# Kernel tuning notes

Hardware: AMD Instinct MI355X
Metric: run time of the kernel (lower is better)

## Reference

```python
import jax, jax.numpy as jnp
import numpy as np

N_NODES = 100000
N_EDGES = 1600000
D_IN = 128
UNITS = 128


def setup_inputs() -> dict:
    key = jax.random.key(0)
    k1, k2, k3, k4, k5 = jax.random.split(key, 5)
    x = jax.random.normal(k1, (N_NODES, D_IN), dtype=jnp.float32)
    # glorot-uniform-like dense weight
    limit = float(np.sqrt(6.0 / (D_IN + UNITS)))
    w = jax.random.uniform(k2, (D_IN, UNITS), minval=-limit, maxval=limit, dtype=jnp.float32)
    # COO sparse adjacency: A[row, col] = val
    edge_row = jax.random.randint(k3, (N_EDGES,), 0, N_NODES, dtype=jnp.int32)
    edge_col = jax.random.randint(k4, (N_EDGES,), 0, N_NODES, dtype=jnp.int32)
    edge_val = jax.random.uniform(k5, (N_EDGES,), dtype=jnp.float32)
    return {"x": x, "w": w, "edge_row": edge_row, "edge_col": edge_col, "edge_val": edge_val}


def reference(x, w, edge_row, edge_col, edge_val):
    # dropout rate = 0.0 -> identity (module default)
    xw = x @ w                                   # [N, units] dense projection
    # sparse adjacency propagation: out[i] = sum_e val[e] * xw[col[e]] for row[e]==i
    msgs = xw[edge_col] * edge_val[:, None]      # [E, units] irregular gather
    out = jax.ops.segment_sum(msgs, edge_row, num_segments=x.shape[0])
    return jax.nn.relu(out)                      # activation
```

## Files before the change

### kernel.cpp

```cpp
#include <hip/hip_runtime.h>

#define N_NODES 100000
#define N_EDGES 1600000
#define D 128
#define NB 512
#define BCAP 3584
#define BSTRIDE 16
#define CHUNK 4000
#define NSCAT 400
#define NGEMMB 521
#define NTILES 1563
#define HCAPQ 1024
#define CTS 132

typedef __attribute__((ext_vector_type(8))) short  short8;
typedef __attribute__((ext_vector_type(4))) float  floatx4;

__device__ __forceinline__ ushort f2bf(float f) {
    unsigned u = __float_as_uint(f);
    u += 0x7FFF + ((u >> 16) & 1);
    return (ushort)(u >> 16);
}
__device__ __forceinline__ float bf2f(ushort s) {
    return __uint_as_float((unsigned)s << 16);
}
__device__ __forceinline__ int bucket_of(int r)  { return (int)(((unsigned)r << 9) / 100000u); }
__device__ __forceinline__ int row_start(int b)  { return (b * 100000 + 511) >> 9; }

union SMem {
    struct {
        int2  stage[CHUNK];
        int   sA[NB];
        int   sB[NB];
        int   lcur[NB];
        int   gbase[NB];
        short sbuck[CHUNK];
    } sc;
    struct {
        ushort wt[128 * 128];
        ushort ct[4][16 * CTS];
    } ge;
};

__global__ __launch_bounds__(256) void gemm_and_scatter(const float* __restrict__ x,
                                                        const float* __restrict__ w,
                                                        ushort* __restrict__ xwb,
                                                        const int* __restrict__ erow,
                                                        const int* __restrict__ ecol,
                                                        const float* __restrict__ eval,
                                                        int* __restrict__ bcnt,
                                                        int2* __restrict__ bkt) {
    __shared__ SMem sm;
    const int t = threadIdx.x;

    if (blockIdx.x < NGEMMB) {
        ushort* wt = sm.ge.wt;
        const int wv   = t >> 6;
        const int lane = t & 63;
        const int m    = lane & 15;
        const int q    = lane >> 4;

        {
            const float4* w4 = (const float4*)w;
            for (int i = t; i < 4096; i += 256) {
                const float4 v = w4[i];
                const int k = i >> 5;
                const int n = (i & 31) << 2;
                const int c = k >> 3, kc = k & 7;
#pragma unroll
                for (int d = 0; d < 4; ++d) {
                    const float val = (d == 0) ? v.x : (d == 1) ? v.y : (d == 2) ? v.z : v.w;
                    const int nn = n + d;
                    wt[(nn << 7) | (((c ^ (nn & 15)) & 15) << 3) | kc] = f2bf(val);
                }
            }
        }
        __syncthreads();

        float4 xa[8];
        {
            const int rb0 = blockIdx.x * 64 + wv * 16;
            const float* xr = x + (size_t)min(rb0 + m, N_NODES - 1) * D + q * 8;
#pragma unroll
            for (int k2 = 0; k2 < 4; ++k2) {
                xa[k2 * 2 + 0] = *(const float4*)(xr + k2 * 32);
                xa[k2 * 2 + 1] = *(const float4*)(xr + k2 * 32 + 4);
            }
        }

        for (int tb = blockIdx.x; tb < NTILES; tb += NGEMMB) {
            const int rbase = tb * 64 + wv * 16;

            short8 afr[4];
#pragma unroll
            for (int k2 = 0; k2 < 4; ++k2) {
                const float4 a0 = xa[k2 * 2 + 0];
                const float4 a1 = xa[k2 * 2 + 1];
                short8 a;
                a[0] = (short)f2bf(a0.x); a[1] = (short)f2bf(a0.y);
                a[2] = (short)f2bf(a0.z); a[3] = (short)f2bf(a0.w);
                a[4] = (short)f2bf(a1.x); a[5] = (short)f2bf(a1.y);
                a[6] = (short)f2bf(a1.z); a[7] = (short)f2bf(a1.w);
                afr[k2] = a;
            }

            const int tnext = tb + NGEMMB;
            if (tnext < NTILES) {
                const int rbn = tnext * 64 + wv * 16;
                const float* xr = x + (size_t)min(rbn + m, N_NODES - 1) * D + q * 8;
#pragma unroll
                for (int k2 = 0; k2 < 4; ++k2) {
                    xa[k2 * 2 + 0] = *(const float4*)(xr + k2 * 32);
                    xa[k2 * 2 + 1] = *(const float4*)(xr + k2 * 32 + 4);
                }
            }

            floatx4 acc[8];
#pragma unroll
            for (int tt = 0; tt < 8; ++tt) acc[tt] = (floatx4){0.f, 0.f, 0.f, 0.f};

#pragma unroll
            for (int k2 = 0; k2 < 4; ++k2) {
#pragma unroll
                for (int tt = 0; tt < 8; ++tt) {
                    const int n  = tt * 16 + m;
                    const int cc = (((k2 << 2) + q) ^ m) & 15;
                    const short8 b = *(const short8*)&wt[(n << 7) | (cc << 3)];
                    acc[tt] = __builtin_amdgcn_mfma_f32_16x16x32_bf16(afr[k2], b, acc[tt], 0, 0, 0);
                }
            }

#pragma unroll
            for (int tt = 0; tt < 8; ++tt) {
#pragma unroll
                for (int r = 0; r < 4; ++r) {
                    sm.ge.ct[wv][((q << 2) | r) * CTS + tt * 16 + m] = f2bf(acc[tt][r]);
                }
            }
            const int rl  = lane >> 2;
            const int ch  = lane & 3;
            const int row = rbase + rl;
            if (row < N_NODES) {
                const ushort* srcp = &sm.ge.ct[wv][rl * CTS + ch * 32];
                ushort*       dstp = &xwb[(size_t)row * D + ch * 32];
#pragma unroll
                for (int u = 0; u < 4; ++u) {
                    ((int4*)dstp)[u] = ((const int4*)srcp)[u];
                }
            }
        }
    } else {
        const int e0 = (blockIdx.x - NGEMMB) * CHUNK;
        int*   sA    = sm.sc.sA;
        int*   sB    = sm.sc.sB;
        int*   lcur  = sm.sc.lcur;
        int*   gbase = sm.sc.gbase;
        short* sbuck = sm.sc.sbuck;
        int2*  stage = sm.sc.stage;

        sA[t] = 0; sA[t + 256] = 0;
        __syncthreads();

        for (int i = t; i < CHUNK; i += 256) {
            atomicAdd(&sA[bucket_of(erow[e0 + i])], 1);
        }
        __syncthreads();

        int cur = 0;
        int* bufs[2] = {sA, sB};
#pragma unroll
        for (int o = 1; o < 512; o <<= 1) {
            const int* src = bufs[cur];
            int*       dst = bufs[cur ^ 1];
            const int i0 = t, i1 = t + 256;
            dst[i0] = src[i0] + ((i0 >= o) ? src[i0 - o] : 0);
            dst[i1] = src[i1] + ((i1 >= o) ? src[i1 - o] : 0);
            cur ^= 1;
            __syncthreads();
        }
        {
            const int* incl = bufs[cur];
            int*       excl = bufs[cur ^ 1];
            excl[t]       = (t == 0) ? 0 : incl[t - 1];
            excl[t + 256] = incl[t + 255];
        }
        __syncthreads();
        int* L = bufs[cur ^ 1];

        for (int b = t; b < NB; b += 256) {
            lcur[b] = L[b];
            const int cnt = ((b == NB - 1) ? CHUNK : L[b + 1]) - L[b];
            gbase[b] = (cnt > 0) ? atomicAdd(&bcnt[b * BSTRIDE], cnt) : 0;
        }
        __syncthreads();

        for (int i = t; i < CHUNK; i += 256) {
            const int   r = erow[e0 + i];
            const int   c = ecol[e0 + i];
            const float v = eval[e0 + i];
            const int   b = bucket_of(r);
            const int  rl = r - row_start(b);
            const int pos = atomicAdd(&lcur[b], 1);
            stage[pos] = make_int2((rl << 17) | c, __float_as_int(v));
            sbuck[pos] = (short)b;
        }
        __syncthreads();

        for (int i = t; i < CHUNK; i += 256) {
            const int b   = sbuck[i];
            const int dst = gbase[b] + (i - L[b]);
            if (dst < BCAP) bkt[(size_t)b * BCAP + dst] = stage[i];
        }
    }
}

__global__ __launch_bounds__(256, 4) void csr_gather(const int* __restrict__ bcnt,
                                                     const int2* __restrict__ bkt,
                                                     const ushort* __restrict__ xwb,
                                                     float* __restrict__ out,
                                                     int b0) {
    __shared__ int2 lcsr[HCAPQ];
    __shared__ int  sA[256], sB[256], lcur[256];
    const int b  = b0 + (blockIdx.x >> 2);
    const int qh = blockIdx.x & 3;
    const int t  = threadIdx.x;
    const int n  = min(bcnt[b * BSTRIDE], BCAP);
    const int r0    = row_start(b);
    const int nrows = row_start(b + 1) - r0;
    const int lo    = (nrows * qh) >> 2;
    const int hi    = (nrows * (qh + 1)) >> 2;
    const int nloc  = hi - lo;

    const int2* src = bkt + (size_t)b * BCAP;
    sA[t] = 0;
    __syncthreads();

    for (int i = t; i < n; i += 256) {
        const int rl = (int)(((unsigned)src[i].x) >> 17);
        if (rl >= lo && rl < hi) atomicAdd(&sA[rl - lo], 1);
    }
    __syncthreads();

    int cur = 0;
    int* bufs[2] = {sA, sB};
#pragma unroll
    for (int o = 1; o < 256; o <<= 1) {
        const int* s = bufs[cur];
        int*       d = bufs[cur ^ 1];
        d[t] = s[t] + ((t >= o) ? s[t - o] : 0);
        cur ^= 1;
        __syncthreads();
    }
    lcur[t] = (t == 0) ? 0 : bufs[cur][t - 1];
    __syncthreads();

    for (int i = t; i < n; i += 256) {
        const int2 e = src[i];
        const int rl = (int)(((unsigned)e.x) >> 17);
        if (rl >= lo && rl < hi) {
            const int pos = atomicAdd(&lcur[rl - lo], 1);
            if (pos < HCAPQ) lcsr[pos] = make_int2(e.x & 0x1FFFF, e.y);
        }
    }
    __syncthreads();

    const int qid = t >> 4;
    const int lc  = (t & 15) << 3;

    for (int ln = qid; ln < nloc; ln += 16) {
        int start = (ln == 0) ? 0 : lcur[ln - 1];
        int end   = lcur[ln];
        start = min(start, HCAPQ);
        end   = min(end, HCAPQ);

        float acc[8] = {0, 0, 0, 0, 0, 0, 0, 0};

        for (int j = start; j < end; j += 4) {
            const int jb = j + 1, jc = j + 2, jd = j + 3;
            const int2 e0 = lcsr[j];
            const int2 e1 = lcsr[min(jb, end - 1)];
            const int2 e2 = lcsr[min(jc, end - 1)];
            const int2 e3 = lcsr[min(jd, end - 1)];
            const short8 m0 = *(const short8*)&xwb[(size_t)e0.x * D + lc];
            const short8 m1 = *(const short8*)&xwb[(size_t)e1.x * D + lc];
            const short8 m2 = *(const short8*)&xwb[(size_t)e2.x * D + lc];
            const short8 m3 = *(const short8*)&xwb[(size_t)e3.x * D + lc];
            const float v0 = __int_as_float(e0.y);
            const float v1 = (jb < end) ? __int_as_float(e1.y) : 0.f;
            const float v2 = (jc < end) ? __int_as_float(e2.y) : 0.f;
            const float v3 = (jd < end) ? __int_as_float(e3.y) : 0.f;
#pragma unroll
            for (int i = 0; i < 8; ++i) {
                acc[i] += v0 * bf2f((ushort)m0[i]);
                acc[i] += v1 * bf2f((ushort)m1[i]);
                acc[i] += v2 * bf2f((ushort)m2[i]);
                acc[i] += v3 * bf2f((ushort)m3[i]);
            }
        }

        float* o = out + (size_t)(r0 + lo + ln) * D + lc;
        *(float4*)(o + 0) = make_float4(fmaxf(acc[0], 0.f), fmaxf(acc[1], 0.f),
                                        fmaxf(acc[2], 0.f), fmaxf(acc[3], 0.f));
        *(float4*)(o + 4) = make_float4(fmaxf(acc[4], 0.f), fmaxf(acc[5], 0.f),
                                        fmaxf(acc[6], 0.f), fmaxf(acc[7], 0.f));
    }
}

extern "C" void kernel_launch(void* const* d_in, const int* in_sizes, int n_in,
                              void* d_out, int out_size, void* d_ws, size_t ws_size,
                              hipStream_t stream) {
    const float* x    = (const float*)d_in[0];
    const float* w    = (const float*)d_in[1];
    const int*   erow = (const int*)d_in[2];
    const int*   ecol = (const int*)d_in[3];
    const float* eval = (const float*)d_in[4];
    float*       out  = (float*)d_out;

    char*   ws_base = (char*)d_ws;
    ushort* xwb  = (ushort*)ws_base;
    int*    bcnt = (int*)(ws_base + 25600000);
    int2*   bkt  = (int2*)(ws_base + 25632768);

    (void)hipMemsetAsync(bcnt, 0, 32768, stream);

    gemm_and_scatter<<<NGEMMB + NSCAT, 256, 0, stream>>>(x, w, xwb, erow, ecol, eval, bcnt, bkt);
    csr_gather<<<1024, 256, 0, stream>>>(bcnt, bkt, xwb, out, 0);
    csr_gather<<<1024, 256, 0, stream>>>(bcnt, bkt, xwb, out, 256);
}
```

Before: 228.6 us.

## Split fused GEMM/scatter kernel into separate launches with swizzled output staging

```diff
diff --git a/kernel.cpp b/kernel.cpp
--- a/kernel.cpp
+++ b/kernel.cpp
@@ -6,12 +6,11 @@
 #define NB 512
 #define BCAP 3584
 #define BSTRIDE 16
-#define CHUNK 4000
-#define NSCAT 400
+#define CHUNK 3200
+#define NSCAT 500
 #define NGEMMB 521
 #define NTILES 1563
 #define HCAPQ 1024
-#define CTS 132
 
 typedef __attribute__((ext_vector_type(8))) short  short8;
 typedef __attribute__((ext_vector_type(4))) float  floatx4;
@@ -27,60 +26,67 @@
 __device__ __forceinline__ int bucket_of(int r)  { return (int)(((unsigned)r << 9) / 100000u); }
 __device__ __forceinline__ int row_start(int b)  { return (b * 100000 + 511) >> 9; }
 
-union SMem {
-    struct {
-        int2  stage[CHUNK];
-        int   sA[NB];
-        int   sB[NB];
-        int   lcur[NB];
-        int   gbase[NB];
-        short sbuck[CHUNK];
-    } sc;
-    struct {
-        ushort wt[128 * 128];
-        ushort ct[4][16 * CTS];
-    } ge;
-};
-
-__global__ __launch_bounds__(256) void gemm_and_scatter(const float* __restrict__ x,
-                                                        const float* __restrict__ w,
-                                                        ushort* __restrict__ xwb,
-                                                        const int* __restrict__ erow,
-                                                        const int* __restrict__ ecol,
-                                                        const float* __restrict__ eval,
-                                                        int* __restrict__ bcnt,
-                                                        int2* __restrict__ bkt) {
-    __shared__ SMem sm;
-    const int t = threadIdx.x;
-
-    if (blockIdx.x < NGEMMB) {
-        ushort* wt = sm.ge.wt;
-        const int wv   = t >> 6;
-        const int lane = t & 63;
-        const int m    = lane & 15;
-        const int q    = lane >> 4;
-
-        {
-            const float4* w4 = (const float4*)w;
-            for (int i = t; i < 4096; i += 256) {
-                const float4 v = w4[i];
-                const int k = i >> 5;
-                const int n = (i & 31) << 2;
-                const int c = k >> 3, kc = k & 7;
-#pragma unroll
-                for (int d = 0; d < 4; ++d) {
-                    const float val = (d == 0) ? v.x : (d == 1) ? v.y : (d == 2) ? v.z : v.w;
-                    const int nn = n + d;
-                    wt[(nn << 7) | (((c ^ (nn & 15)) & 15) << 3) | kc] = f2bf(val);
-                }
-            }
-        }
-        __syncthreads();
-
-        float4 xa[8];
-        {
-            const int rb0 = blockIdx.x * 64 + wv * 16;
-            const float* xr = x + (size_t)min(rb0 + m, N_NODES - 1) * D + q * 8;
+__global__ __launch_bounds__(256) void gemm_xw(const float* __restrict__ x,
+                                               const float* __restrict__ w,
+                                               ushort* __restrict__ xwb) {
+    __shared__ ushort wt[128 * 128];
+    __shared__ ushort ct[4][16 * 64];
+    const int t    = threadIdx.x;
+    const int wv   = t >> 6;
+    const int lane = t & 63;
+    const int m    = lane & 15;
+    const int q    = lane >> 4;
+
+    {
+        const float4* w4 = (const float4*)w;
+        const int kb    = t & 7;
+        const int ncol4 = t >> 3;
+        const int n     = ncol4 << 2;
+        for (int it = 0; it < 16; ++it) {
+            const int k = kb + it * 8;
+            const float4 v = w4[k * 32 + ncol4];
+            const int c = k >> 3, kc = k & 7;
+#pragma unroll
+            for (int d = 0; d < 4; ++d) {
+                const float val = (d == 0) ? v.x : (d == 1) ? v.y : (d == 2) ? v.z : v.w;
+                const int nn = n + d;
+                wt[(nn << 7) | (((c ^ (nn & 15)) & 15) << 3) | kc] = f2bf(val);
+            }
+        }
+    }
+    __syncthreads();
+
+    float4 xa[8];
+    {
+        const int rb0 = blockIdx.x * 64 + wv * 16;
+        const float* xr = x + (size_t)min(rb0 + m, N_NODES - 1) * D + q * 8;
+#pragma unroll
+        for (int k2 = 0; k2 < 4; ++k2) {
+            xa[k2 * 2 + 0] = *(const float4*)(xr + k2 * 32);
+            xa[k2 * 2 + 1] = *(const float4*)(xr + k2 * 32 + 4);
+        }
+    }
+
+    for (int tb = blockIdx.x; tb < NTILES; tb += NGEMMB) {
+        const int rbase = tb * 64 + wv * 16;
+
+        short8 afr[4];
+#pragma unroll
+        for (int k2 = 0; k2 < 4; ++k2) {
+            const float4 a0 = xa[k2 * 2 + 0];
+            const float4 a1 = xa[k2 * 2 + 1];
+            short8 a;
+            a[0] = (short)f2bf(a0.x); a[1] = (short)f2bf(a0.y);
+            a[2] = (short)f2bf(a0.z); a[3] = (short)f2bf(a0.w);
+            a[4] = (short)f2bf(a1.x); a[5] = (short)f2bf(a1.y);
+            a[6] = (short)f2bf(a1.z); a[7] = (short)f2bf(a1.w);
+            afr[k2] = a;
+        }
+
+        const int tnext = tb + NGEMMB;
+        if (tnext < NTILES) {
+            const int rbn = tnext * 64 + wv * 16;
+            const float* xr = x + (size_t)min(rbn + m, N_NODES - 1) * D + q * 8;
 #pragma unroll
             for (int k2 = 0; k2 < 4; ++k2) {
                 xa[k2 * 2 + 0] = *(const float4*)(xr + k2 * 32);
@@ -88,129 +94,108 @@
             }
         }
 
-        for (int tb = blockIdx.x; tb < NTILES; tb += NGEMMB) {
-            const int rbase = tb * 64 + wv * 16;
-
-            short8 afr[4];
-#pragma unroll
-            for (int k2 = 0; k2 < 4; ++k2) {
-                const float4 a0 = xa[k2 * 2 + 0];
-                const float4 a1 = xa[k2 * 2 + 1];
-                short8 a;
-                a[0] = (short)f2bf(a0.x); a[1] = (short)f2bf(a0.y);
-                a[2] = (short)f2bf(a0.z); a[3] = (short)f2bf(a0.w);
-                a[4] = (short)f2bf(a1.x); a[5] = (short)f2bf(a1.y);
-                a[6] = (short)f2bf(a1.z); a[7] = (short)f2bf(a1.w);
-                afr[k2] = a;
-            }
-
-            const int tnext = tb + NGEMMB;
-            if (tnext < NTILES) {
-                const int rbn = tnext * 64 + wv * 16;
-                const float* xr = x + (size_t)min(rbn + m, N_NODES - 1) * D + q * 8;
-#pragma unroll
-                for (int k2 = 0; k2 < 4; ++k2) {
-                    xa[k2 * 2 + 0] = *(const float4*)(xr + k2 * 32);
-                    xa[k2 * 2 + 1] = *(const float4*)(xr + k2 * 32 + 4);
+        floatx4 acc[8];
+#pragma unroll
+        for (int tt = 0; tt < 8; ++tt) acc[tt] = (floatx4){0.f, 0.f, 0.f, 0.f};
+
+#pragma unroll
+        for (int k2 = 0; k2 < 4; ++k2) {
+#pragma unroll
+            for (int tt = 0; tt < 8; ++tt) {
+                const int n  = tt * 16 + m;
+                const int cc = (((k2 << 2) + q) ^ m) & 15;
+                const short8 b = *(const short8*)&wt[(n << 7) | (cc << 3)];
+                acc[tt] = __builtin_amdgcn_mfma_f32_16x16x32_bf16(afr[k2], b, acc[tt], 0, 0, 0);
+            }
+        }
+
+#pragma unroll
+        for (int p = 0; p < 2; ++p) {
+#pragma unroll
+            for (int tt2 = 0; tt2 < 4; ++tt2) {
+#pragma unroll
+                for (int r = 0; r < 4; ++r) {
+                    const int row  = (q << 2) | r;
+                    const int slot = (tt2 ^ r ^ q) & 3;
+                    ct[wv][row * 64 + slot * 16 + m] = f2bf(acc[p * 4 + tt2][r]);
                 }
             }
-
-            floatx4 acc[8];
-#pragma unroll
-            for (int tt = 0; tt < 8; ++tt) acc[tt] = (floatx4){0.f, 0.f, 0.f, 0.f};
-
-#pragma unroll
-            for (int k2 = 0; k2 < 4; ++k2) {
-#pragma unroll
-                for (int tt = 0; tt < 8; ++tt) {
-                    const int n  = tt * 16 + m;
-                    const int cc = (((k2 << 2) + q) ^ m) & 15;
-                    const short8 b = *(const short8*)&wt[(n << 7) | (cc << 3)];
-                    acc[tt] = __builtin_amdgcn_mfma_f32_16x16x32_bf16(afr[k2], b, acc[tt], 0, 0, 0);
-                }
-            }
-
-#pragma unroll
-            for (int tt = 0; tt < 8; ++tt) {
-#pragma unroll
-                for (int r = 0; r < 4; ++r) {
-                    sm.ge.ct[wv][((q << 2) | r) * CTS + tt * 16 + m] = f2bf(acc[tt][r]);
-                }
-            }
-            const int rl  = lane >> 2;
-            const int ch  = lane & 3;
-            const int row = rbase + rl;
-            if (row < N_NODES) {
-                const ushort* srcp = &sm.ge.ct[wv][rl * CTS + ch * 32];
-                ushort*       dstp = &xwb[(size_t)row * D + ch * 32];
-#pragma unroll
-                for (int u = 0; u < 4; ++u) {
-                    ((int4*)dstp)[u] = ((const int4*)srcp)[u];
-                }
-            }
-        }
-    } else {
-        const int e0 = (blockIdx.x - NGEMMB) * CHUNK;
-        int*   sA    = sm.sc.sA;
-        int*   sB    = sm.sc.sB;
-        int*   lcur  = sm.sc.lcur;
-        int*   gbase = sm.sc.gbase;
-        short* sbuck = sm.sc.sbuck;
-        int2*  stage = sm.sc.stage;
-
-        sA[t] = 0; sA[t + 256] = 0;
+            const int rl   = lane >> 2;
+            const int ch   = lane & 3;
+            const int slot = (ch ^ (rl & 3) ^ (rl >> 2)) & 3;
+            const ushort* srcp = &ct[wv][rl * 64 + slot * 16];
+            if (rbase + rl < N_NODES) {
+                ushort* dstp = &xwb[(size_t)(rbase + rl) * D + p * 64 + ch * 16];
+                ((int4*)dstp)[0] = ((const int4*)srcp)[0];
+                ((int4*)dstp)[1] = ((const int4*)srcp)[1];
+            }
+        }
+    }
+}
+
+__global__ __launch_bounds__(256) void bucket_scatter(const int* __restrict__ erow,
+                                                      const int* __restrict__ ecol,
+                                                      const float* __restrict__ eval,
+                                                      int* __restrict__ bcnt,
+                                                      int2* __restrict__ bkt) {
+    __shared__ int2  stage[CHUNK];
+    __shared__ int   sA[NB], sB[NB], lcur[NB], gbase[NB];
+    __shared__ short sbuck[CHUNK];
+    const int t  = threadIdx.x;
+    const int e0 = blockIdx.x * CHUNK;
+
+    sA[t] = 0; sA[t + 256] = 0;
+    __syncthreads();
+
+    for (int i = t; i < CHUNK; i += 256) {
+        atomicAdd(&sA[bucket_of(erow[e0 + i])], 1);
+    }
+    __syncthreads();
+
+    int cur = 0;
+    int* bufs[2] = {sA, sB};
+#pragma unroll
+    for (int o = 1; o < 512; o <<= 1) {
+        const int* src = bufs[cur];
+        int*       dst = bufs[cur ^ 1];
+        const int i0 = t, i1 = t + 256;
+        dst[i0] = src[i0] + ((i0 >= o) ? src[i0 - o] : 0);
+        dst[i1] = src[i1] + ((i1 >= o) ? src[i1 - o] : 0);
+        cur ^= 1;
         __syncthreads();
-
-        for (int i = t; i < CHUNK; i += 256) {
-            atomicAdd(&sA[bucket_of(erow[e0 + i])], 1);
-        }
-        __syncthreads();
-
-        int cur = 0;
-        int* bufs[2] = {sA, sB};
-#pragma unroll
-        for (int o = 1; o < 512; o <<= 1) {
-            const int* src = bufs[cur];
-            int*       dst = bufs[cur ^ 1];
-            const int i0 = t, i1 = t + 256;
-            dst[i0] = src[i0] + ((i0 >= o) ? src[i0 - o] : 0);
-            dst[i1] = src[i1] + ((i1 >= o) ? src[i1 - o] : 0);
-            cur ^= 1;
-            __syncthreads();
-        }
-        {
-            const int* incl = bufs[cur];
-            int*       excl = bufs[cur ^ 1];
-            excl[t]       = (t == 0) ? 0 : incl[t - 1];
-            excl[t + 256] = incl[t + 255];
-        }
-        __syncthreads();
-        int* L = bufs[cur ^ 1];
-
-        for (int b = t; b < NB; b += 256) {
-            lcur[b] = L[b];
-            const int cnt = ((b == NB - 1) ? CHUNK : L[b + 1]) - L[b];
-            gbase[b] = (cnt > 0) ? atomicAdd(&bcnt[b * BSTRIDE], cnt) : 0;
-        }
-        __syncthreads();
-
-        for (int i = t; i < CHUNK; i += 256) {
-            const int   r = erow[e0 + i];
-            const int   c = ecol[e0 + i];
-            const float v = eval[e0 + i];
-            const int   b = bucket_of(r);
-            const int  rl = r - row_start(b);
-            const int pos = atomicAdd(&lcur[b], 1);
-            stage[pos] = make_int2((rl << 17) | c, __float_as_int(v));
-            sbuck[pos] = (short)b;
-        }
-        __syncthreads();
-
-        for (int i = t; i < CHUNK; i += 256) {
-            const int b   = sbuck[i];
-            const int dst = gbase[b] + (i - L[b]);
-            if (dst < BCAP) bkt[(size_t)b * BCAP + dst] = stage[i];
-        }
+    }
+    {
+        const int* incl = bufs[cur];
+        int*       excl = bufs[cur ^ 1];
+        excl[t]       = (t == 0) ? 0 : incl[t - 1];
+        excl[t + 256] = incl[t + 255];
+    }
+    __syncthreads();
+    int* L = bufs[cur ^ 1];
+
+    for (int b = t; b < NB; b += 256) {
+        lcur[b] = L[b];
+        const int cnt = ((b == NB - 1) ? CHUNK : L[b + 1]) - L[b];
+        gbase[b] = (cnt > 0) ? atomicAdd(&bcnt[b * BSTRIDE], cnt) : 0;
+    }
+    __syncthreads();
+
+    for (int i = t; i < CHUNK; i += 256) {
+        const int   r = erow[e0 + i];
+        const int   c = ecol[e0 + i];
+        const float v = eval[e0 + i];
+        const int   b = bucket_of(r);
+        const int  rl = r - row_start(b);
+        const int pos = atomicAdd(&lcur[b], 1);
+        stage[pos] = make_int2((rl << 17) | c, __float_as_int(v));
+        sbuck[pos] = (short)b;
+    }
+    __syncthreads();
+
+    for (int i = t; i < CHUNK; i += 256) {
+        const int b   = sbuck[i];
+        const int dst = gbase[b] + (i - L[b]);
+        if (dst < BCAP) bkt[(size_t)b * BCAP + dst] = stage[i];
     }
 }
 
@@ -323,7 +308,8 @@
 
     (void)hipMemsetAsync(bcnt, 0, 32768, stream);
 
-    gemm_and_scatter<<<NGEMMB + NSCAT, 256, 0, stream>>>(x, w, xwb, erow, ecol, eval, bcnt, bkt);
+    gemm_xw<<<NGEMMB, 256, 0, stream>>>(x, w, xwb);
+    bucket_scatter<<<NSCAT, 256, 0, stream>>>(erow, ecol, eval, bcnt, bkt);
     csr_gather<<<1024, 256, 0, stream>>>(bcnt, bkt, xwb, out, 0);
     csr_gather<<<1024, 256, 0, stream>>>(bcnt, bkt, xwb, out, 256);
 }
```

Result: slower. 237.5 us (+3.9%).
